# Kernel tuning notes

Hardware: AMD Instinct MI355X
Metric: run time of the kernel (lower is better)

## Reference

```python
import jax, jax.numpy as jnp
import numpy as np

N_NODES = 100000
N_EDGES = 1600000
D_IN = 64
D_OUT = 64


def setup_inputs() -> dict:
    key = jax.random.key(0)
    k1, k2, k3 = jax.random.split(key, 3)
    edge_index = jax.random.randint(k1, (2, N_EDGES), 0, N_NODES, dtype=jnp.int64)
    x = jax.random.normal(k2, (N_NODES, D_IN), dtype=jnp.float32)
    W = jax.random.normal(k3, (D_OUT, D_IN), dtype=jnp.float32) * (1.0 / np.sqrt(D_IN))
    return {"edge_index": edge_index, "x": x, "W": W}


def reference(edge_index, x, W):
    # GCN forward: h = W x, then out = D^{-1/2} A D^{-1/2} h (symmetric normalization
    # of the COO edge list, matching normalize_edge_index + CSR SpMM in the original).
    N = x.shape[0]
    row, col = edge_index[0], edge_index[1]
    # degree from row occurrences of the adjacency
    deg = jax.ops.segment_sum(jnp.ones(row.shape, x.dtype), row, num_segments=N)
    dinv_sqrt = jnp.where(deg > 0, 1.0 / jnp.sqrt(deg), 0.0)
    w = dinv_sqrt[row] * dinv_sqrt[col]  # [E] edge weights
    xh = x @ W.T                          # dense linear, bias=False  [N, D_OUT]
    # SpMM: out[r] = sum_e w_e * xh[col_e] for edges with row_e == r
    out = jax.ops.segment_sum(w[:, None] * xh[col], row, num_segments=N)
    return out
```

## Files before the change

kernel.cpp:

```cpp
#include <hip/hip_runtime.h>
#include <hip/hip_fp16.h>

#define D     64
#define RPB   256
#define BCAP  4608
#define EPB   4096
#define NBMAX 400

typedef __attribute__((ext_vector_type(8))) _Float16 f16x8;
typedef __attribute__((ext_vector_type(4))) float    f32x4;

__global__ __launch_bounds__(256) void bucket_kernel(const int* __restrict__ ei, int E,
                                                     int nb,
                                                     int* __restrict__ cursor,
                                                     int* __restrict__ bbuf) {
    __shared__ int hist[NBMAX];
    __shared__ int base_l[NBMAX];
    __shared__ int stage_v[EPB];
    __shared__ unsigned short stage_b[EPB];
    int tid = threadIdx.x;

    for (int i = tid; i < nb; i += 256) hist[i] = 0;
    __syncthreads();

    long long e0 = (long long)blockIdx.x * EPB;
#pragma unroll
    for (int i = 0; i < EPB / 256; ++i) {
        int idx = i * 256 + tid;
        long long e = e0 + idx;
        unsigned short b = 0xFFFF;
        int v = 0;
        if (e < E) {
            int r = ei[e];
            int c = ei[E + e];
            b = (unsigned short)(r >> 8);
            v = ((r & (RPB - 1)) << 17) | c;
            atomicAdd(&hist[b], 1);
        }
        stage_v[idx] = v;
        stage_b[idx] = b;
    }
    __syncthreads();

    for (int i = tid; i < nb; i += 256) {
        int c = hist[i];
        base_l[i] = (c > 0) ? atomicAdd(&cursor[i], c) : 0;
        hist[i] = 0;
    }
    __syncthreads();

#pragma unroll
    for (int i = 0; i < EPB / 256; ++i) {
        int idx = i * 256 + tid;
        unsigned short b = stage_b[idx];
        if (b != 0xFFFF) {
            int off = base_l[b] + atomicAdd(&hist[b], 1);
            if (off < BCAP)
                bbuf[(size_t)b * BCAP + off] = stage_v[idx];
        }
    }
}

__global__ __launch_bounds__(256) void sort_kernel(const int* __restrict__ cursor,
                                                   int* __restrict__ bbuf,
                                                   float* __restrict__ dinv,
                                                   int2* __restrict__ rowinfo, int N) {
    __shared__ int sorted[BCAP];
    __shared__ int hist[RPB];
    __shared__ int pfx[RPB];
    __shared__ int curs[RPB];
    int b = blockIdx.x, tid = threadIdx.x;
    int cnt = min(cursor[b], BCAP);
    int* gbuf = bbuf + (size_t)b * BCAP;

    hist[tid] = 0;
    __syncthreads();
    for (int j = tid; j < cnt; j += 256) atomicAdd(&hist[gbuf[j] >> 17], 1);
    __syncthreads();

    int dv = hist[tid];
    pfx[tid] = dv;
    __syncthreads();
    for (int off = 1; off < 256; off <<= 1) {
        int add = (tid >= off) ? pfx[tid - off] : 0;
        __syncthreads();
        pfx[tid] += add;
        __syncthreads();
    }
    int excl = pfx[tid] - dv;

    int r = (b << 8) + tid;
    if (r < N) {
        dinv[r] = (dv > 0) ? rsqrtf((float)dv) : 0.0f;
        rowinfo[r] = make_int2(b * BCAP + excl, dv);
    }
    curs[tid] = excl;
    __syncthreads();

    for (int j = tid; j < cnt; j += 256) {
        int v = gbuf[j];
        int pos = atomicAdd(&curs[v >> 17], 1);
        sorted[pos] = v;
    }
    __syncthreads();
    for (int j = tid; j < cnt; j += 256) gbuf[j] = sorted[j];
}

__global__ __launch_bounds__(256) void linear_kernel(const float* __restrict__ x,
                                                     const float* __restrict__ W,
                                                     const float* __restrict__ dinv,
                                                     __half* __restrict__ xh, int M) {
    int tid  = threadIdx.x;
    int lane = tid & 63;
    int wv   = tid >> 6;
    int r16  = lane & 15;
    int quad = lane >> 4;

    if (blockIdx.x == 0 && tid < D) xh[(size_t)M * D + tid] = __float2half(0.0f);

    f16x8 Bf[4][2];
#pragma unroll
    for (int g = 0; g < 4; ++g)
#pragma unroll
        for (int s = 0; s < 2; ++s) {
            const float4* wp = (const float4*)(W + (size_t)(16 * g + r16) * D + 32 * s + quad * 8);
            float4 w0 = wp[0], w1 = wp[1];
            f16x8 h;
            h[0] = (_Float16)w0.x; h[1] = (_Float16)w0.y;
            h[2] = (_Float16)w0.z; h[3] = (_Float16)w0.w;
            h[4] = (_Float16)w1.x; h[5] = (_Float16)w1.y;
            h[6] = (_Float16)w1.z; h[7] = (_Float16)w1.w;
            Bf[g][s] = h;
        }

    int ntiles = (M + 15) / 16;
    int stride = gridDim.x * 4;
    for (int t = blockIdx.x * 4 + wv; t < ntiles; t += stride) {
        int r0 = t * 16;
        int ra = min(r0 + r16, M - 1);
        const float4* xp = (const float4*)(x + (size_t)ra * D + quad * 8);
        float4 a0 = xp[0], a1 = xp[1], a2 = xp[8], a3 = xp[9];
        f16x8 A0, A1;
        A0[0] = (_Float16)a0.x; A0[1] = (_Float16)a0.y; A0[2] = (_Float16)a0.z; A0[3] = (_Float16)a0.w;
        A0[4] = (_Float16)a1.x; A0[5] = (_Float16)a1.y; A0[6] = (_Float16)a1.z; A0[7] = (_Float16)a1.w;
        A1[0] = (_Float16)a2.x; A1[1] = (_Float16)a2.y; A1[2] = (_Float16)a2.z; A1[3] = (_Float16)a2.w;
        A1[4] = (_Float16)a3.x; A1[5] = (_Float16)a3.y; A1[6] = (_Float16)a3.z; A1[7] = (_Float16)a3.w;

        f32x4 acc[4];
#pragma unroll
        for (int g = 0; g < 4; ++g) {
            f32x4 z = {0.f, 0.f, 0.f, 0.f};
            z = __builtin_amdgcn_mfma_f32_16x16x32_f16(A0, Bf[g][0], z, 0, 0, 0);
            acc[g] = __builtin_amdgcn_mfma_f32_16x16x32_f16(A1, Bf[g][1], z, 0, 0, 0);
        }

#pragma unroll
        for (int reg = 0; reg < 4; ++reg) {
            int rr = r0 + quad * 4 + reg;
            if (rr < M) {
                float dvr = dinv[rr];
                __half* op = xh + (size_t)rr * D + r16;
#pragma unroll
                for (int g = 0; g < 4; ++g)
                    op[16 * g] = __float2half(dvr * acc[g][reg]);
            }
        }
    }
}

__global__ __launch_bounds__(256) void spmm_kernel(const int2* __restrict__ rowinfo,
                                                   const int* __restrict__ bbuf,
                                                   const float* __restrict__ dinv,
                                                   const __half2* __restrict__ xh2,
                                                   float2* __restrict__ out2, int N) {
    int r = (blockIdx.x * 256 + threadIdx.x) >> 6;
    if (r >= N) return;
    int c   = threadIdx.x & 63;
    int sub = c >> 5;
    int f   = c & 31;

    int2 ri   = rowinfo[r];
    int start = ri.x;
    int d     = ri.y;
    float dr  = dinv[r];

    float ax = 0.f, ay = 0.f;
    for (int j0 = 0; j0 < d; j0 += 64) {
        int n = d - j0;
        if (n > 64) n = 64;
        int cn_reg = (c < n) ? (bbuf[start + j0 + c] & 0x1FFFF) : N;
        int n8 = (n + 7) & ~7;
        for (int k = 0; k < n8; k += 8) {
            int e0 = __shfl(cn_reg, k + 0 + sub);
            int e1 = __shfl(cn_reg, k + 2 + sub);
            int e2 = __shfl(cn_reg, k + 4 + sub);
            int e3 = __shfl(cn_reg, k + 6 + sub);
            float2 v0 = __half22float2(xh2[(size_t)e0 * 32 + f]);
            float2 v1 = __half22float2(xh2[(size_t)e1 * 32 + f]);
            float2 v2 = __half22float2(xh2[(size_t)e2 * 32 + f]);
            float2 v3 = __half22float2(xh2[(size_t)e3 * 32 + f]);
            ax += (v0.x + v1.x) + (v2.x + v3.x);
            ay += (v0.y + v1.y) + (v2.y + v3.y);
        }
    }
    float sx = ax + __shfl(ax, c ^ 32);
    float sy = ay + __shfl(ay, c ^ 32);
    if (sub == 0) {
        out2[(size_t)r * 32 + f] = make_float2(dr * sx, dr * sy);
    }
}

extern "C" void kernel_launch(void* const* d_in, const int* in_sizes, int n_in,
                              void* d_out, int out_size, void* d_ws, size_t ws_size,
                              hipStream_t stream) {
    const int*   ei = (const int*)d_in[0];
    const float* x  = (const float*)d_in[1];
    const float* W  = (const float*)d_in[2];
    float* out = (float*)d_out;

    int E  = in_sizes[0] / 2;
    int N  = in_sizes[1] / D;
    int nb = (N + RPB - 1) / RPB;

    char* p = (char*)d_ws;
    size_t off = 0;
    auto take = [&](size_t bytes) -> char* {
        char* cur = p + off;
        off = (off + bytes + 255) & ~(size_t)255;
        return cur;
    };
    float*  dinv    = (float*)take((size_t)N * 4);
    int2*   rowinfo = (int2*)take((size_t)N * 8);
    int*    cursor  = (int*)take((size_t)nb * 4);
    int*    bbuf    = (int*)take((size_t)nb * BCAP * 4);
    __half* xh      = (__half*)take((size_t)(N + 1) * D * 2);
    (void)ws_size;

    hipMemsetAsync(cursor, 0, (size_t)nb * 4, stream);

    bucket_kernel<<<(E + EPB - 1) / EPB, 256, 0, stream>>>(ei, E, nb, cursor, bbuf);
    sort_kernel<<<nb, 256, 0, stream>>>(cursor, bbuf, dinv, rowinfo, N);
    linear_kernel<<<1024, 256, 0, stream>>>(x, W, dinv, xh, N);
    spmm_kernel<<<(N + 3) / 4, 256, 0, stream>>>(rowinfo, bbuf, dinv,
                                                 (const __half2*)xh, (float2*)out, N);
}
```

Measured before the change: 167.1 us.

## Tune bucketing block size, widen sort blocks, unroll SpMM gathers, nontemporal stores

Halves the edges handled per bucket block so more blocks run, and launches the sort kernel with 512 threads while guarding the per-row histogram and scan to the first 256. The SpMM inner loop now issues eight gathered loads per iteration instead of four, raising memory-level parallelism, and writes its output with nontemporal stores. In exchange, rows with few edges do more wasted padding work, since groups of 16 are padded to the dummy zero row, and the bucket kernel makes more global atomic calls on the cursor array.

```diff
diff --git a/kernel.cpp b/kernel.cpp
--- a/kernel.cpp
+++ b/kernel.cpp
@@ -4,7 +4,7 @@
 #define D     64
 #define RPB   256
 #define BCAP  4608
-#define EPB   4096
+#define EPB   2048
 #define NBMAX 400
 
 typedef __attribute__((ext_vector_type(8))) _Float16 f16x8;
@@ -61,7 +61,7 @@
     }
 }
 
-__global__ __launch_bounds__(256) void sort_kernel(const int* __restrict__ cursor,
+__global__ __launch_bounds__(512) void sort_kernel(const int* __restrict__ cursor,
                                                    int* __restrict__ bbuf,
                                                    float* __restrict__ dinv,
                                                    int2* __restrict__ rowinfo, int N) {
@@ -73,37 +73,40 @@
     int cnt = min(cursor[b], BCAP);
     int* gbuf = bbuf + (size_t)b * BCAP;
 
-    hist[tid] = 0;
-    __syncthreads();
-    for (int j = tid; j < cnt; j += 256) atomicAdd(&hist[gbuf[j] >> 17], 1);
-    __syncthreads();
-
-    int dv = hist[tid];
-    pfx[tid] = dv;
-    __syncthreads();
-    for (int off = 1; off < 256; off <<= 1) {
-        int add = (tid >= off) ? pfx[tid - off] : 0;
+    if (tid < RPB) hist[tid] = 0;
+    __syncthreads();
+    for (int j = tid; j < cnt; j += 512) atomicAdd(&hist[gbuf[j] >> 17], 1);
+    __syncthreads();
+
+    int dv = 0;
+    if (tid < RPB) { dv = hist[tid]; pfx[tid] = dv; }
+    __syncthreads();
+    for (int off = 1; off < RPB; off <<= 1) {
+        int add = 0;
+        if (tid < RPB && tid >= off) add = pfx[tid - off];
         __syncthreads();
-        pfx[tid] += add;
+        if (tid < RPB) pfx[tid] += add;
         __syncthreads();
     }
-    int excl = pfx[tid] - dv;
-
-    int r = (b << 8) + tid;
-    if (r < N) {
-        dinv[r] = (dv > 0) ? rsqrtf((float)dv) : 0.0f;
-        rowinfo[r] = make_int2(b * BCAP + excl, dv);
-    }
-    curs[tid] = excl;
-    __syncthreads();
-
-    for (int j = tid; j < cnt; j += 256) {
+
+    if (tid < RPB) {
+        int excl = pfx[tid] - dv;
+        int r = (b << 8) + tid;
+        if (r < N) {
+            dinv[r] = (dv > 0) ? rsqrtf((float)dv) : 0.0f;
+            rowinfo[r] = make_int2(b * BCAP + excl, dv);
+        }
+        curs[tid] = excl;
+    }
+    __syncthreads();
+
+    for (int j = tid; j < cnt; j += 512) {
         int v = gbuf[j];
         int pos = atomicAdd(&curs[v >> 17], 1);
         sorted[pos] = v;
     }
     __syncthreads();
-    for (int j = tid; j < cnt; j += 256) gbuf[j] = sorted[j];
+    for (int j = tid; j < cnt; j += 512) gbuf[j] = sorted[j];
 }
 
 __global__ __launch_bounds__(256) void linear_kernel(const float* __restrict__ x,
@@ -189,24 +192,34 @@
         int n = d - j0;
         if (n > 64) n = 64;
         int cn_reg = (c < n) ? (bbuf[start + j0 + c] & 0x1FFFF) : N;
-        int n8 = (n + 7) & ~7;
-        for (int k = 0; k < n8; k += 8) {
-            int e0 = __shfl(cn_reg, k + 0 + sub);
-            int e1 = __shfl(cn_reg, k + 2 + sub);
-            int e2 = __shfl(cn_reg, k + 4 + sub);
-            int e3 = __shfl(cn_reg, k + 6 + sub);
+        int n16 = (n + 15) & ~15;
+        for (int k = 0; k < n16; k += 16) {
+            int e0 = __shfl(cn_reg, k +  0 + sub);
+            int e1 = __shfl(cn_reg, k +  2 + sub);
+            int e2 = __shfl(cn_reg, k +  4 + sub);
+            int e3 = __shfl(cn_reg, k +  6 + sub);
+            int e4 = __shfl(cn_reg, k +  8 + sub);
+            int e5 = __shfl(cn_reg, k + 10 + sub);
+            int e6 = __shfl(cn_reg, k + 12 + sub);
+            int e7 = __shfl(cn_reg, k + 14 + sub);
             float2 v0 = __half22float2(xh2[(size_t)e0 * 32 + f]);
             float2 v1 = __half22float2(xh2[(size_t)e1 * 32 + f]);
             float2 v2 = __half22float2(xh2[(size_t)e2 * 32 + f]);
             float2 v3 = __half22float2(xh2[(size_t)e3 * 32 + f]);
-            ax += (v0.x + v1.x) + (v2.x + v3.x);
-            ay += (v0.y + v1.y) + (v2.y + v3.y);
+            float2 v4 = __half22float2(xh2[(size_t)e4 * 32 + f]);
+            float2 v5 = __half22float2(xh2[(size_t)e5 * 32 + f]);
+            float2 v6 = __half22float2(xh2[(size_t)e6 * 32 + f]);
+            float2 v7 = __half22float2(xh2[(size_t)e7 * 32 + f]);
+            ax += ((v0.x + v1.x) + (v2.x + v3.x)) + ((v4.x + v5.x) + (v6.x + v7.x));
+            ay += ((v0.y + v1.y) + (v2.y + v3.y)) + ((v4.y + v5.y) + (v6.y + v7.y));
         }
     }
     float sx = ax + __shfl(ax, c ^ 32);
     float sy = ay + __shfl(ay, c ^ 32);
     if (sub == 0) {
-        out2[(size_t)r * 32 + f] = make_float2(dr * sx, dr * sy);
+        float2 res = make_float2(dr * sx, dr * sy);
+        __builtin_nontemporal_store(__builtin_bit_cast(double, res),
+                                    (double*)&out2[(size_t)r * 32 + f]);
     }
 }
 
@@ -239,7 +252,7 @@
     hipMemsetAsync(cursor, 0, (size_t)nb * 4, stream);
 
     bucket_kernel<<<(E + EPB - 1) / EPB, 256, 0, stream>>>(ei, E, nb, cursor, bbuf);
-    sort_kernel<<<nb, 256, 0, stream>>>(cursor, bbuf, dinv, rowinfo, N);
+    sort_kernel<<<nb, 512, 0, stream>>>(cursor, bbuf, dinv, rowinfo, N);
     linear_kernel<<<1024, 256, 0, stream>>>(x, W, dinv, xh, N);
     spmm_kernel<<<(N + 3) / 4, 256, 0, stream>>>(rowinfo, bbuf, dinv,
                                                  (const __half2*)xh, (float2*)out, N);
```

Result: no change. 166.0 us (-0.7%).
